# Performance work log

Measured on AMD Instinct MI355X. Metric: run time of the kernel, lower is better.

## Reference

```python
import jax, jax.numpy as jnp
import numpy as np

U, N, E, D = 200000, 50000, 1600000, 64


def setup_inputs() -> dict:
    key = jax.random.key(0)
    ks = jax.random.split(key, 8)
    nodes = jax.random.randint(ks[0], (N,), 0, U)
    neigh_idx = jax.random.randint(ks[1], (E,), 0, U)
    seg_ids = jnp.sort(jax.random.randint(ks[2], (E,), 0, N))
    u2e = jax.random.normal(ks[3], (U, D), dtype=jnp.float32) * 0.1
    W1 = jax.random.normal(ks[4], (2 * D, D), dtype=jnp.float32) * 0.1
    b1 = jnp.zeros((D,), dtype=jnp.float32)
    W2 = jax.random.normal(ks[5], (D, D), dtype=jnp.float32) * 0.1
    b2 = jnp.zeros((D,), dtype=jnp.float32)
    w3 = jax.random.normal(ks[6], (D, 1), dtype=jnp.float32) * 0.1
    b3 = jnp.zeros((1,), dtype=jnp.float32)
    return {"nodes": nodes, "neigh_idx": neigh_idx, "seg_ids": seg_ids,
            "u2e": u2e, "W1": W1, "b1": b1, "W2": W2, "b2": b2,
            "w3": w3, "b3": b3}


def reference(nodes, neigh_idx, seg_ids, u2e, W1, b1, W2, b2, w3, b3):
    # Per-node self representation  [N, D]
    u_rep = u2e[nodes]
    # Ragged neighbor gather flattened to edge list
    e_u = u2e[neigh_idx]                      # [E, D]
    u_edge = u_rep[seg_ids]                   # [E, D] node rep broadcast to its edges
    # Attention MLP (GraphRec-style), eval mode (no dropout)
    x = jnp.concatenate([e_u, u_edge], axis=1)            # [E, 2D]
    x = jax.nn.relu(x @ W1 + b1)
    x = jax.nn.relu(x @ W2 + b2)
    logits = (x @ w3 + b3)[:, 0]                           # [E]
    # Segment softmax over each node's neighbor set
    seg_max = jax.ops.segment_max(logits, seg_ids, num_segments=N)
    ex = jnp.exp(logits - seg_max[seg_ids])
    denom = jax.ops.segment_sum(ex, seg_ids, num_segments=N)
    att = ex / denom[seg_ids]                              # [E]
    # Attention-weighted neighbor aggregation: e_u^T @ att per node
    agg = jax.ops.segment_sum(att[:, None] * e_u, seg_ids, num_segments=N)  # [N, D]
    # Nodes with zero neighbors fall back to their own embedding
    counts = jax.ops.segment_sum(jnp.ones((E,), dtype=jnp.float32), seg_ids, num_segments=N)
    out = jnp.where(counts[:, None] > 0, agg, u_rep)
    return out
```

## Files before the change

### kernel.cpp

```cpp
#include <hip/hip_runtime.h>
#include <math.h>

#define D 64

typedef __fp16 fp16x2 __attribute__((ext_vector_type(2)));
typedef _Float16 half8 __attribute__((ext_vector_type(8)));
typedef __attribute__((ext_vector_type(4))) float f32x4;

union h8pun { half8 v; fp16x2 h2[4]; };

__global__ __launch_bounds__(256) void k_prep(const float* __restrict__ W1,
                                              const float* __restrict__ W2,
                                              float* __restrict__ W1at,
                                              float* __restrict__ W1bt,
                                              float* __restrict__ W2t,
                                              const int* __restrict__ seg_ids,
                                              int* __restrict__ start, int E, int N) {
    int i = blockIdx.x * 256 + threadIdx.x;
    if (i < 3 * D * D) {
        int mat = i / (D * D), j = i % (D * D);
        int r = j >> 6, c = j & 63;
        if (mat == 0)      W1at[c * D + r] = W1[r * D + c];
        else if (mat == 1) W1bt[c * D + r] = W1[(D + r) * D + c];
        else               W2t[c * D + r] = W2[r * D + c];
    }
    if (i <= N) {
        int lo = 0, hi = E;
        while (lo < hi) {
            int mid = (lo + hi) >> 1;
            if (seg_ids[mid] < i) lo = mid + 1; else hi = mid;
        }
        start[i] = lo;
    }
}

__global__ __launch_bounds__(256) void k_proj_both(const float* __restrict__ u2e,
                                                   const int* __restrict__ nodes,
                                                   const float* __restrict__ W1at,
                                                   const float* __restrict__ W1bt,
                                                   const float* __restrict__ b1,
                                                   _Float16* __restrict__ q,
                                                   _Float16* __restrict__ u2e_h,
                                                   _Float16* __restrict__ p,
                                                   int U, int N, int wavesU, int wavesN) {
    int lane = threadIdx.x & 63;
    int m = lane & 15, quad = lane >> 4;
    int wave = (blockIdx.x * blockDim.x + threadIdx.x) >> 6;

    const float* Wt;
    const int* idx;
    const float* bias;
    _Float16* outp;
    _Float16* copyp;
    int R, w0, wstride;
    if (wave < wavesU) {
        Wt = W1at; idx = nullptr; bias = nullptr; outp = q; copyp = u2e_h;
        R = U; w0 = wave; wstride = wavesU;
    } else {
        Wt = W1bt; idx = nodes; bias = b1; outp = p; copyp = nullptr;
        R = N; w0 = wave - wavesU; wstride = wavesN;
    }

    half8 Bf[2][4];
    float bv[4];
#pragma unroll
    for (int t = 0; t < 4; ++t) {
        int n = m + 16 * t;
        bv[t] = bias ? bias[n] : 0.0f;
#pragma unroll
        for (int kh = 0; kh < 2; ++kh) {
            const float* col = Wt + n * D + kh * 32 + quad * 8;
#pragma unroll
            for (int j = 0; j < 8; ++j) Bf[kh][t][j] = (_Float16)col[j];
        }
    }

    int ngroups = (R + 15) / 16;
    for (int g = w0; g < ngroups; g += wstride) {
        int r_ = g * 16 + m;
        int rs = r_ < R ? r_ : R - 1;
        int src = idx ? idx[rs] : rs;
        const float4* arow = (const float4*)(u2e + (size_t)src * D);
        float4 x0 = arow[quad * 2], x1 = arow[quad * 2 + 1];
        float4 y0 = arow[8 + quad * 2], y1 = arow[8 + quad * 2 + 1];
        h8pun A0, A1;
        A0.h2[0] = __builtin_amdgcn_cvt_pkrtz(x0.x, x0.y);
        A0.h2[1] = __builtin_amdgcn_cvt_pkrtz(x0.z, x0.w);
        A0.h2[2] = __builtin_amdgcn_cvt_pkrtz(x1.x, x1.y);
        A0.h2[3] = __builtin_amdgcn_cvt_pkrtz(x1.z, x1.w);
        A1.h2[0] = __builtin_amdgcn_cvt_pkrtz(y0.x, y0.y);
        A1.h2[1] = __builtin_amdgcn_cvt_pkrtz(y0.z, y0.w);
        A1.h2[2] = __builtin_amdgcn_cvt_pkrtz(y1.x, y1.y);
        A1.h2[3] = __builtin_amdgcn_cvt_pkrtz(y1.z, y1.w);
        if (copyp && r_ < R) {
            *(half8*)(copyp + (size_t)r_ * D + quad * 8) = A0.v;
            *(half8*)(copyp + (size_t)r_ * D + 32 + quad * 8) = A1.v;
        }
        f32x4 C[4];
#pragma unroll
        for (int t = 0; t < 4; ++t) C[t] = (f32x4){bv[t], bv[t], bv[t], bv[t]};
#pragma unroll
        for (int t = 0; t < 4; ++t) {
            C[t] = __builtin_amdgcn_mfma_f32_16x16x32_f16(A0.v, Bf[0][t], C[t], 0, 0, 0);
            C[t] = __builtin_amdgcn_mfma_f32_16x16x32_f16(A1.v, Bf[1][t], C[t], 0, 0, 0);
        }
#pragma unroll
        for (int r = 0; r < 4; ++r) {
            int row = g * 16 + quad * 4 + r;
            if (row < R) {
#pragma unroll
                for (int t = 0; t < 4; ++t)
                    outp[(size_t)row * D + m + 16 * t] = (_Float16)C[t][r];
            }
        }
    }
}

__global__ __launch_bounds__(256) void k_edge_logits_mfma(const int* __restrict__ neigh_idx,
                                                          const int* __restrict__ seg_ids,
                                                          const _Float16* __restrict__ q,
                                                          const _Float16* __restrict__ p,
                                                          const float* __restrict__ W2t,
                                                          const float* __restrict__ b2,
                                                          const float* __restrict__ w3,
                                                          const float* __restrict__ b3,
                                                          float* __restrict__ logits, int E) {
    int lane = threadIdx.x & 63;
    int m = lane & 15, quad = lane >> 4;

    half8 Bf[2][4];
    float b2v[4], w3v[4];
#pragma unroll
    for (int t = 0; t < 4; ++t) {
        int n = m + 16 * t;
        b2v[t] = b2[n];
        w3v[t] = w3[n];
#pragma unroll
        for (int kh = 0; kh < 2; ++kh) {
            const float* col = W2t + n * D + kh * 32 + quad * 8;
#pragma unroll
            for (int j = 0; j < 8; ++j) Bf[kh][t][j] = (_Float16)col[j];
        }
    }
    float b3v = b3[0];
    const half8 hz = {0, 0, 0, 0, 0, 0, 0, 0};

    int ngroups = (E + 31) / 32;
    int wave = (blockIdx.x * blockDim.x + threadIdx.x) >> 6;
    int nwaves = (gridDim.x * blockDim.x) >> 6;

    half8 cqa0 = hz, cqa1 = hz, cpa0 = hz, cpa1 = hz;
    half8 cqb0 = hz, cqb1 = hz, cpb0 = hz, cpb1 = hz;
    int g = wave;
    if (g < ngroups) {
        int ea = g * 32 + m, eb = ea + 16;
        int eas = ea < E ? ea : E - 1;
        int ebs = eb < E ? eb : E - 1;
        int nbra = neigh_idx[eas], sega = seg_ids[eas];
        int nbrb = neigh_idx[ebs], segb = seg_ids[ebs];
        const half8* qra = (const half8*)(q + (size_t)nbra * D);
        const half8* pra = (const half8*)(p + (size_t)sega * D);
        const half8* qrb = (const half8*)(q + (size_t)nbrb * D);
        const half8* prb = (const half8*)(p + (size_t)segb * D);
        cqa0 = qra[quad]; cqa1 = qra[quad + 4];
        cpa0 = pra[quad]; cpa1 = pra[quad + 4];
        cqb0 = qrb[quad]; cqb1 = qrb[quad + 4];
        cpb0 = prb[quad]; cpb1 = prb[quad + 4];
    }
    for (; g < ngroups; g += nwaves) {
        int gn = g + nwaves;
        int gs = gn < ngroups ? gn : g;
        int ea2 = gs * 32 + m, eb2 = ea2 + 16;
        int eas2 = ea2 < E ? ea2 : E - 1;
        int ebs2 = eb2 < E ? eb2 : E - 1;
        int nbra2 = neigh_idx[eas2], sega2 = seg_ids[eas2];
        int nbrb2 = neigh_idx[ebs2], segb2 = seg_ids[ebs2];
        half8 Aa0 = __builtin_elementwise_max(cqa0 + cpa0, hz);
        half8 Aa1 = __builtin_elementwise_max(cqa1 + cpa1, hz);
        half8 Ab0 = __builtin_elementwise_max(cqb0 + cpb0, hz);
        half8 Ab1 = __builtin_elementwise_max(cqb1 + cpb1, hz);
        const half8* qra2 = (const half8*)(q + (size_t)nbra2 * D);
        const half8* pra2 = (const half8*)(p + (size_t)sega2 * D);
        const half8* qrb2 = (const half8*)(q + (size_t)nbrb2 * D);
        const half8* prb2 = (const half8*)(p + (size_t)segb2 * D);
        half8 nqa0 = qra2[quad], nqa1 = qra2[quad + 4];
        half8 npa0 = pra2[quad], npa1 = pra2[quad + 4];
        half8 nqb0 = qrb2[quad], nqb1 = qrb2[quad + 4];
        half8 npb0 = prb2[quad], npb1 = prb2[quad + 4];
        f32x4 Ca[4], Cb[4];
#pragma unroll
        for (int t = 0; t < 4; ++t) {
            Ca[t] = (f32x4){b2v[t], b2v[t], b2v[t], b2v[t]};
            Cb[t] = Ca[t];
        }
#pragma unroll
        for (int t = 0; t < 4; ++t) {
            Ca[t] = __builtin_amdgcn_mfma_f32_16x16x32_f16(Aa0, Bf[0][t], Ca[t], 0, 0, 0);
            Ca[t] = __builtin_amdgcn_mfma_f32_16x16x32_f16(Aa1, Bf[1][t], Ca[t], 0, 0, 0);
            Cb[t] = __builtin_amdgcn_mfma_f32_16x16x32_f16(Ab0, Bf[0][t], Cb[t], 0, 0, 0);
            Cb[t] = __builtin_amdgcn_mfma_f32_16x16x32_f16(Ab1, Bf[1][t], Cb[t], 0, 0, 0);
        }
        float pa[4], pb[4];
#pragma unroll
        for (int r = 0; r < 4; ++r) {
            float sa = 0.0f, sb = 0.0f;
#pragma unroll
            for (int t = 0; t < 4; ++t) {
                sa += fmaxf(Ca[t][r], 0.0f) * w3v[t];
                sb += fmaxf(Cb[t][r], 0.0f) * w3v[t];
            }
            pa[r] = sa; pb[r] = sb;
        }
#pragma unroll
        for (int off = 1; off <= 8; off <<= 1) {
#pragma unroll
            for (int r = 0; r < 4; ++r) {
                pa[r] += __shfl_xor(pa[r], off, 64);
                pb[r] += __shfl_xor(pb[r], off, 64);
            }
        }
        if (m == 0) {
            int e0 = g * 32 + quad * 4;
            if (e0 + 3 < E)
                *(float4*)(logits + e0) = make_float4(pa[0] + b3v, pa[1] + b3v, pa[2] + b3v, pa[3] + b3v);
            else
#pragma unroll
                for (int r = 0; r < 4; ++r)
                    if (e0 + r < E) logits[e0 + r] = pa[r] + b3v;
            int e1 = e0 + 16;
            if (e1 + 3 < E)
                *(float4*)(logits + e1) = make_float4(pb[0] + b3v, pb[1] + b3v, pb[2] + b3v, pb[3] + b3v);
            else
#pragma unroll
                for (int r = 0; r < 4; ++r)
                    if (e1 + r < E) logits[e1 + r] = pb[r] + b3v;
        }
        cqa0 = nqa0; cqa1 = nqa1; cpa0 = npa0; cpa1 = npa1;
        cqb0 = nqb0; cqb1 = nqb1; cpb0 = npb0; cpb1 = npb1;
    }
}

__global__ __launch_bounds__(256) void k_agg(const int* __restrict__ nodes,
                                             const int* __restrict__ neigh_idx,
                                             const float* __restrict__ u2e,
                                             const _Float16* __restrict__ u2e_h,
                                             const float* __restrict__ logits,
                                             const int* __restrict__ start,
                                             float* __restrict__ out, int N) {
    int n = blockIdx.x * 4 + ((int)threadIdx.x >> 6);
    int lane = threadIdx.x & 63;
    if (n >= N) return;
    int s = start[n];
    int t = start[n + 1];
    if (s == t) {
        int node = nodes[n];
        out[(size_t)n * D + lane] = u2e[(size_t)node * D + lane];
        return;
    }
    float mx = -INFINITY;
    for (int i = s + lane; i < t; i += 64) mx = fmaxf(mx, logits[i]);
#pragma unroll
    for (int off = 32; off >= 1; off >>= 1) mx = fmaxf(mx, __shfl_xor(mx, off, 64));
    float ssum = 0.0f;
    for (int i = s + lane; i < t; i += 64) ssum += __expf(logits[i] - mx);
#pragma unroll
    for (int off = 32; off >= 1; off >>= 1) ssum += __shfl_xor(ssum, off, 64);
    float inv = 1.0f / ssum;

    int grp = lane >> 3, sub = lane & 7;
    float acc[8];
#pragma unroll
    for (int j = 0; j < 8; ++j) acc[j] = 0.0f;
    for (int i = s; i < t; i += 32) {
#pragma unroll
        for (int uu = 0; uu < 4; ++uu) {
            int ii = i + uu * 8 + grp;
            bool v = ii < t;
            int is = v ? ii : s;
            float lg = logits[is];
            int nb = neigh_idx[is];
            half8 r = *(const half8*)(u2e_h + (size_t)nb * D + sub * 8);
            float a = v ? __expf(lg - mx) * inv : 0.0f;
#pragma unroll
            for (int j = 0; j < 8; ++j) acc[j] += a * (float)r[j];
        }
    }
#pragma unroll
    for (int off = 8; off <= 32; off <<= 1) {
#pragma unroll
        for (int j = 0; j < 8; ++j) acc[j] += __shfl_xor(acc[j], off, 64);
    }
    if (grp == 0) {
        float* o = out + (size_t)n * D + sub * 8;
        *(float4*)o = make_float4(acc[0], acc[1], acc[2], acc[3]);
        *(float4*)(o + 4) = make_float4(acc[4], acc[5], acc[6], acc[7]);
    }
}

extern "C" void kernel_launch(void* const* d_in, const int* in_sizes, int n_in,
                              void* d_out, int out_size, void* d_ws, size_t ws_size,
                              hipStream_t stream) {
    const int* nodes = (const int*)d_in[0];
    const int* neigh_idx = (const int*)d_in[1];
    const int* seg_ids = (const int*)d_in[2];
    const float* u2e = (const float*)d_in[3];
    const float* W1 = (const float*)d_in[4];
    const float* b1 = (const float*)d_in[5];
    const float* W2 = (const float*)d_in[6];
    const float* b2 = (const float*)d_in[7];
    const float* w3 = (const float*)d_in[8];
    const float* b3 = (const float*)d_in[9];
    float* out = (float*)d_out;

    int N = in_sizes[0];
    int E = in_sizes[1];
    int U = in_sizes[3] / D;

    char* ws = (char*)d_ws;
    size_t off = 0;
    auto alloc = [&](size_t bytes) {
        void* ptr = ws + off;
        off = (off + bytes + 255) & ~(size_t)255;
        return ptr;
    };
    float* logits = (float*)alloc((size_t)E * 4);
    int* start = (int*)alloc((size_t)(N + 1) * 4);
    float* W1at = (float*)alloc((size_t)D * D * 4);
    float* W1bt = (float*)alloc((size_t)D * D * 4);
    float* W2t = (float*)alloc((size_t)D * D * 4);
    _Float16* q = (_Float16*)alloc((size_t)U * D * 2);
    _Float16* p = (_Float16*)alloc((size_t)N * D * 2);
    _Float16* u2e_h = (_Float16*)alloc((size_t)U * D * 2);
    (void)ws_size;

    int prep_n = (N + 1) > 3 * D * D ? (N + 1) : 3 * D * D;
    k_prep<<<(prep_n + 255) / 256, 256, 0, stream>>>(W1, W2, W1at, W1bt, W2t,
                                                     seg_ids, start, E, N);
    const int wavesU = 4096, wavesN = 1024;
    k_proj_both<<<(wavesU + wavesN) / 4, 256, 0, stream>>>(u2e, nodes, W1at, W1bt, b1,
                                                           q, u2e_h, p, U, N, wavesU, wavesN);
    k_edge_logits_mfma<<<2048, 256, 0, stream>>>(neigh_idx, seg_ids, q, p, W2t,
                                                 b2, w3, b3, logits, E);
    k_agg<<<(N + 3) / 4, 256, 0, stream>>>(nodes, neigh_idx, u2e, u2e_h, logits, start, out, N);
}
```

Before: 247.1 us.

## Fuse edge logits, online segment softmax and aggregation into one per-node kernel

Merges the edge-logit MLP kernel and the aggregation kernel into a single per-node kernel. Each wave walks its node's edges in chunks of 16 and keeps a running max and sum so the softmax is computed online, which removes the logits buffer and the second pass over edges. The fp16 embedding copy and its W1 projection are interleaved into one 128-wide row, so each neighbor's data sits in a single contiguous row. The b3 bias is dropped, which is valid because softmax is shift-invariant. In exchange, edges are processed per node with partially filled 16-edge tiles, which can waste MFMA work and hurt load balance on uneven degrees.

Measured after the change: 254.7 us. 1.03x slower.

```diff
diff --git a/kernel.cpp b/kernel.cpp
--- a/kernel.cpp
+++ b/kernel.cpp
@@ -5,6 +5,7 @@
 
 typedef __fp16 fp16x2 __attribute__((ext_vector_type(2)));
 typedef _Float16 half8 __attribute__((ext_vector_type(8)));
+typedef _Float16 half4v __attribute__((ext_vector_type(4)));
 typedef __attribute__((ext_vector_type(4))) float f32x4;
 
 union h8pun { half8 v; fp16x2 h2[4]; };
@@ -39,8 +40,7 @@
                                                    const float* __restrict__ W1at,
                                                    const float* __restrict__ W1bt,
                                                    const float* __restrict__ b1,
-                                                   _Float16* __restrict__ q,
-                                                   _Float16* __restrict__ u2e_h,
+                                                   _Float16* __restrict__ ue,
                                                    _Float16* __restrict__ p,
                                                    int U, int N, int wavesU, int wavesN) {
     int lane = threadIdx.x & 63;
@@ -52,12 +52,14 @@
     const float* bias;
     _Float16* outp;
     _Float16* copyp;
-    int R, w0, wstride;
+    int R, w0, wstride, ostride;
     if (wave < wavesU) {
-        Wt = W1at; idx = nullptr; bias = nullptr; outp = q; copyp = u2e_h;
+        Wt = W1at; idx = nullptr; bias = nullptr;
+        outp = ue + D; copyp = ue; ostride = 2 * D;
         R = U; w0 = wave; wstride = wavesU;
     } else {
-        Wt = W1bt; idx = nodes; bias = b1; outp = p; copyp = nullptr;
+        Wt = W1bt; idx = nodes; bias = b1;
+        outp = p; copyp = nullptr; ostride = D;
         R = N; w0 = wave - wavesU; wstride = wavesN;
     }
 
@@ -93,8 +95,8 @@
         A1.h2[2] = __builtin_amdgcn_cvt_pkrtz(y1.x, y1.y);
         A1.h2[3] = __builtin_amdgcn_cvt_pkrtz(y1.z, y1.w);
         if (copyp && r_ < R) {
-            *(half8*)(copyp + (size_t)r_ * D + quad * 8) = A0.v;
-            *(half8*)(copyp + (size_t)r_ * D + 32 + quad * 8) = A1.v;
+            *(half8*)(copyp + (size_t)r_ * 2 * D + quad * 8) = A0.v;
+            *(half8*)(copyp + (size_t)r_ * 2 * D + 32 + quad * 8) = A1.v;
         }
         f32x4 C[4];
 #pragma unroll
@@ -110,21 +112,22 @@
             if (row < R) {
 #pragma unroll
                 for (int t = 0; t < 4; ++t)
-                    outp[(size_t)row * D + m + 16 * t] = (_Float16)C[t][r];
-            }
-        }
-    }
-}
-
-__global__ __launch_bounds__(256) void k_edge_logits_mfma(const int* __restrict__ neigh_idx,
-                                                          const int* __restrict__ seg_ids,
-                                                          const _Float16* __restrict__ q,
-                                                          const _Float16* __restrict__ p,
-                                                          const float* __restrict__ W2t,
-                                                          const float* __restrict__ b2,
-                                                          const float* __restrict__ w3,
-                                                          const float* __restrict__ b3,
-                                                          float* __restrict__ logits, int E) {
+                    outp[(size_t)row * ostride + m + 16 * t] = (_Float16)C[t][r];
+            }
+        }
+    }
+}
+
+__global__ __launch_bounds__(256) void k_fused(const int* __restrict__ nodes,
+                                               const int* __restrict__ neigh_idx,
+                                               const float* __restrict__ u2e,
+                                               const _Float16* __restrict__ ue,
+                                               const _Float16* __restrict__ p,
+                                               const float* __restrict__ W2t,
+                                               const float* __restrict__ b2,
+                                               const float* __restrict__ w3,
+                                               const int* __restrict__ start,
+                                               float* __restrict__ out, int N) {
     int lane = threadIdx.x & 63;
     int m = lane & 15, quad = lane >> 4;
 
@@ -132,168 +135,100 @@
     float b2v[4], w3v[4];
 #pragma unroll
     for (int t = 0; t < 4; ++t) {
-        int n = m + 16 * t;
-        b2v[t] = b2[n];
-        w3v[t] = w3[n];
+        int nn = m + 16 * t;
+        b2v[t] = b2[nn];
+        w3v[t] = w3[nn];
 #pragma unroll
         for (int kh = 0; kh < 2; ++kh) {
-            const float* col = W2t + n * D + kh * 32 + quad * 8;
+            const float* col = W2t + nn * D + kh * 32 + quad * 8;
 #pragma unroll
             for (int j = 0; j < 8; ++j) Bf[kh][t][j] = (_Float16)col[j];
         }
     }
-    float b3v = b3[0];
     const half8 hz = {0, 0, 0, 0, 0, 0, 0, 0};
 
-    int ngroups = (E + 31) / 32;
     int wave = (blockIdx.x * blockDim.x + threadIdx.x) >> 6;
     int nwaves = (gridDim.x * blockDim.x) >> 6;
-
-    half8 cqa0 = hz, cqa1 = hz, cpa0 = hz, cpa1 = hz;
-    half8 cqb0 = hz, cqb1 = hz, cpb0 = hz, cpb1 = hz;
-    int g = wave;
-    if (g < ngroups) {
-        int ea = g * 32 + m, eb = ea + 16;
-        int eas = ea < E ? ea : E - 1;
-        int ebs = eb < E ? eb : E - 1;
-        int nbra = neigh_idx[eas], sega = seg_ids[eas];
-        int nbrb = neigh_idx[ebs], segb = seg_ids[ebs];
-        const half8* qra = (const half8*)(q + (size_t)nbra * D);
-        const half8* pra = (const half8*)(p + (size_t)sega * D);
-        const half8* qrb = (const half8*)(q + (size_t)nbrb * D);
-        const half8* prb = (const half8*)(p + (size_t)segb * D);
-        cqa0 = qra[quad]; cqa1 = qra[quad + 4];
-        cpa0 = pra[quad]; cpa1 = pra[quad + 4];
-        cqb0 = qrb[quad]; cqb1 = qrb[quad + 4];
-        cpb0 = prb[quad]; cpb1 = prb[quad + 4];
-    }
-    for (; g < ngroups; g += nwaves) {
-        int gn = g + nwaves;
-        int gs = gn < ngroups ? gn : g;
-        int ea2 = gs * 32 + m, eb2 = ea2 + 16;
-        int eas2 = ea2 < E ? ea2 : E - 1;
-        int ebs2 = eb2 < E ? eb2 : E - 1;
-        int nbra2 = neigh_idx[eas2], sega2 = seg_ids[eas2];
-        int nbrb2 = neigh_idx[ebs2], segb2 = seg_ids[ebs2];
-        half8 Aa0 = __builtin_elementwise_max(cqa0 + cpa0, hz);
-        half8 Aa1 = __builtin_elementwise_max(cqa1 + cpa1, hz);
-        half8 Ab0 = __builtin_elementwise_max(cqb0 + cpb0, hz);
-        half8 Ab1 = __builtin_elementwise_max(cqb1 + cpb1, hz);
-        const half8* qra2 = (const half8*)(q + (size_t)nbra2 * D);
-        const half8* pra2 = (const half8*)(p + (size_t)sega2 * D);
-        const half8* qrb2 = (const half8*)(q + (size_t)nbrb2 * D);
-        const half8* prb2 = (const half8*)(p + (size_t)segb2 * D);
-        half8 nqa0 = qra2[quad], nqa1 = qra2[quad + 4];
-        half8 npa0 = pra2[quad], npa1 = pra2[quad + 4];
-        half8 nqb0 = qrb2[quad], nqb1 = qrb2[quad + 4];
-        half8 npb0 = prb2[quad], npb1 = prb2[quad + 4];
-        f32x4 Ca[4], Cb[4];
-#pragma unroll
-        for (int t = 0; t < 4; ++t) {
-            Ca[t] = (f32x4){b2v[t], b2v[t], b2v[t], b2v[t]};
-            Cb[t] = Ca[t];
-        }
-#pragma unroll
-        for (int t = 0; t < 4; ++t) {
-            Ca[t] = __builtin_amdgcn_mfma_f32_16x16x32_f16(Aa0, Bf[0][t], Ca[t], 0, 0, 0);
-            Ca[t] = __builtin_amdgcn_mfma_f32_16x16x32_f16(Aa1, Bf[1][t], Ca[t], 0, 0, 0);
-            Cb[t] = __builtin_amdgcn_mfma_f32_16x16x32_f16(Ab0, Bf[0][t], Cb[t], 0, 0, 0);
-            Cb[t] = __builtin_amdgcn_mfma_f32_16x16x32_f16(Ab1, Bf[1][t], Cb[t], 0, 0, 0);
-        }
-        float pa[4], pb[4];
-#pragma unroll
-        for (int r = 0; r < 4; ++r) {
-            float sa = 0.0f, sb = 0.0f;
-#pragma unroll
-            for (int t = 0; t < 4; ++t) {
-                sa += fmaxf(Ca[t][r], 0.0f) * w3v[t];
-                sb += fmaxf(Cb[t][r], 0.0f) * w3v[t];
-            }
-            pa[r] = sa; pb[r] = sb;
-        }
-#pragma unroll
-        for (int off = 1; off <= 8; off <<= 1) {
+    for (int n = wave; n < N; n += nwaves) {
+        int s = start[n];
+        int t = start[n + 1];
+        if (s == t) {
+            int node = nodes[n];
+            out[(size_t)n * D + lane] = u2e[(size_t)node * D + lane];
+            continue;
+        }
+        const half8* prow = (const half8*)(p + (size_t)n * D);
+        half8 pa0 = prow[quad], pa1 = prow[quad + 4];
+        float m_run = -1e30f, ssum = 0.0f;
+        float acc0 = 0.f, acc1 = 0.f, acc2 = 0.f, acc3 = 0.f;
+        for (int base = s; base < t; base += 16) {
+            int e = base + m;
+            int es = e < t ? e : t - 1;
+            int nb = neigh_idx[es];
+            const half8* qrow = (const half8*)(ue + (size_t)nb * (2 * D) + D);
+            half8 qa0 = qrow[quad], qa1 = qrow[quad + 4];
+            half8 A0 = __builtin_elementwise_max(qa0 + pa0, hz);
+            half8 A1 = __builtin_elementwise_max(qa1 + pa1, hz);
+            f32x4 C[4];
+#pragma unroll
+            for (int t4 = 0; t4 < 4; ++t4) C[t4] = (f32x4){b2v[t4], b2v[t4], b2v[t4], b2v[t4]};
+#pragma unroll
+            for (int t4 = 0; t4 < 4; ++t4) {
+                C[t4] = __builtin_amdgcn_mfma_f32_16x16x32_f16(A0, Bf[0][t4], C[t4], 0, 0, 0);
+                C[t4] = __builtin_amdgcn_mfma_f32_16x16x32_f16(A1, Bf[1][t4], C[t4], 0, 0, 0);
+            }
+            float lw[4];
 #pragma unroll
             for (int r = 0; r < 4; ++r) {
-                pa[r] += __shfl_xor(pa[r], off, 64);
-                pb[r] += __shfl_xor(pb[r], off, 64);
-            }
-        }
-        if (m == 0) {
-            int e0 = g * 32 + quad * 4;
-            if (e0 + 3 < E)
-                *(float4*)(logits + e0) = make_float4(pa[0] + b3v, pa[1] + b3v, pa[2] + b3v, pa[3] + b3v);
-            else
-#pragma unroll
-                for (int r = 0; r < 4; ++r)
-                    if (e0 + r < E) logits[e0 + r] = pa[r] + b3v;
-            int e1 = e0 + 16;
-            if (e1 + 3 < E)
-                *(float4*)(logits + e1) = make_float4(pb[0] + b3v, pb[1] + b3v, pb[2] + b3v, pb[3] + b3v);
-            else
-#pragma unroll
-                for (int r = 0; r < 4; ++r)
-                    if (e1 + r < E) logits[e1 + r] = pb[r] + b3v;
-        }
-        cqa0 = nqa0; cqa1 = nqa1; cpa0 = npa0; cpa1 = npa1;
-        cqb0 = nqb0; cqb1 = nqb1; cpb0 = npb0; cpb1 = npb1;
-    }
-}
-
-__global__ __launch_bounds__(256) void k_agg(const int* __restrict__ nodes,
-                                             const int* __restrict__ neigh_idx,
-                                             const float* __restrict__ u2e,
-                                             const _Float16* __restrict__ u2e_h,
-                                             const float* __restrict__ logits,
-                                             const int* __restrict__ start,
-                                             float* __restrict__ out, int N) {
-    int n = blockIdx.x * 4 + ((int)threadIdx.x >> 6);
-    int lane = threadIdx.x & 63;
-    if (n >= N) return;
-    int s = start[n];
-    int t = start[n + 1];
-    if (s == t) {
-        int node = nodes[n];
-        out[(size_t)n * D + lane] = u2e[(size_t)node * D + lane];
-        return;
-    }
-    float mx = -INFINITY;
-    for (int i = s + lane; i < t; i += 64) mx = fmaxf(mx, logits[i]);
-#pragma unroll
-    for (int off = 32; off >= 1; off >>= 1) mx = fmaxf(mx, __shfl_xor(mx, off, 64));
-    float ssum = 0.0f;
-    for (int i = s + lane; i < t; i += 64) ssum += __expf(logits[i] - mx);
-#pragma unroll
-    for (int off = 32; off >= 1; off >>= 1) ssum += __shfl_xor(ssum, off, 64);
-    float inv = 1.0f / ssum;
-
-    int grp = lane >> 3, sub = lane & 7;
-    float acc[8];
-#pragma unroll
-    for (int j = 0; j < 8; ++j) acc[j] = 0.0f;
-    for (int i = s; i < t; i += 32) {
-#pragma unroll
-        for (int uu = 0; uu < 4; ++uu) {
-            int ii = i + uu * 8 + grp;
-            bool v = ii < t;
-            int is = v ? ii : s;
-            float lg = logits[is];
-            int nb = neigh_idx[is];
-            half8 r = *(const half8*)(u2e_h + (size_t)nb * D + sub * 8);
-            float a = v ? __expf(lg - mx) * inv : 0.0f;
-#pragma unroll
-            for (int j = 0; j < 8; ++j) acc[j] += a * (float)r[j];
-        }
-    }
-#pragma unroll
-    for (int off = 8; off <= 32; off <<= 1) {
-#pragma unroll
-        for (int j = 0; j < 8; ++j) acc[j] += __shfl_xor(acc[j], off, 64);
-    }
-    if (grp == 0) {
-        float* o = out + (size_t)n * D + sub * 8;
-        *(float4*)o = make_float4(acc[0], acc[1], acc[2], acc[3]);
-        *(float4*)(o + 4) = make_float4(acc[4], acc[5], acc[6], acc[7]);
+                float sa = 0.0f;
+#pragma unroll
+                for (int t4 = 0; t4 < 4; ++t4)
+                    sa += fmaxf(C[t4][r], 0.0f) * w3v[t4];
+                lw[r] = sa;
+            }
+#pragma unroll
+            for (int off = 1; off <= 8; off <<= 1) {
+#pragma unroll
+                for (int r = 0; r < 4; ++r) lw[r] += __shfl_xor(lw[r], off, 64);
+            }
+#pragma unroll
+            for (int r = 0; r < 4; ++r)
+                if (base + quad * 4 + r >= t) lw[r] = -1e30f;
+            float mc = fmaxf(fmaxf(lw[0], lw[1]), fmaxf(lw[2], lw[3]));
+            mc = fmaxf(mc, __shfl_xor(mc, 16, 64));
+            mc = fmaxf(mc, __shfl_xor(mc, 32, 64));
+            float mnew = fmaxf(m_run, mc);
+            float scale = __expf(m_run - mnew);
+            float w[4];
+            float wsum = 0.0f;
+#pragma unroll
+            for (int r = 0; r < 4; ++r) { w[r] = __expf(lw[r] - mnew); wsum += w[r]; }
+            wsum += __shfl_xor(wsum, 16, 64);
+            wsum += __shfl_xor(wsum, 32, 64);
+            ssum = ssum * scale + wsum;
+            acc0 *= scale; acc1 *= scale; acc2 *= scale; acc3 *= scale;
+#pragma unroll
+            for (int r = 0; r < 4; ++r) {
+                int nbr = __shfl(nb, 4 * quad + r, 64);
+                half4v row = *(const half4v*)(ue + (size_t)nbr * (2 * D) + m * 4);
+                acc0 += w[r] * (float)row[0];
+                acc1 += w[r] * (float)row[1];
+                acc2 += w[r] * (float)row[2];
+                acc3 += w[r] * (float)row[3];
+            }
+            m_run = mnew;
+        }
+#pragma unroll
+        for (int off = 16; off <= 32; off <<= 1) {
+            acc0 += __shfl_xor(acc0, off, 64);
+            acc1 += __shfl_xor(acc1, off, 64);
+            acc2 += __shfl_xor(acc2, off, 64);
+            acc3 += __shfl_xor(acc3, off, 64);
+        }
+        float inv = 1.0f / ssum;
+        if (quad == 0)
+            *(float4*)(out + (size_t)n * D + m * 4) =
+                make_float4(acc0 * inv, acc1 * inv, acc2 * inv, acc3 * inv);
     }
 }
 
@@ -310,6 +245,7 @@
     const float* b2 = (const float*)d_in[7];
     const float* w3 = (const float*)d_in[8];
     const float* b3 = (const float*)d_in[9];
+    (void)b3;
     float* out = (float*)d_out;
 
     int N = in_sizes[0];
@@ -323,14 +259,12 @@
         off = (off + bytes + 255) & ~(size_t)255;
         return ptr;
     };
-    float* logits = (float*)alloc((size_t)E * 4);
     int* start = (int*)alloc((size_t)(N + 1) * 4);
     float* W1at = (float*)alloc((size_t)D * D * 4);
     float* W1bt = (float*)alloc((size_t)D * D * 4);
     float* W2t = (float*)alloc((size_t)D * D * 4);
-    _Float16* q = (_Float16*)alloc((size_t)U * D * 2);
+    _Float16* ue = (_Float16*)alloc((size_t)U * 2 * D * 2);
     _Float16* p = (_Float16*)alloc((size_t)N * D * 2);
-    _Float16* u2e_h = (_Float16*)alloc((size_t)U * D * 2);
     (void)ws_size;
 
     int prep_n = (N + 1) > 3 * D * D ? (N + 1) : 3 * D * D;
@@ -338,8 +272,7 @@
                                                      seg_ids, start, E, N);
     const int wavesU = 4096, wavesN = 1024;
     k_proj_both<<<(wavesU + wavesN) / 4, 256, 0, stream>>>(u2e, nodes, W1at, W1bt, b1,
-                                                           q, u2e_h, p, U, N, wavesU, wavesN);
-    k_edge_logits_mfma<<<2048, 256, 0, stream>>>(neigh_idx, seg_ids, q, p, W2t,
-                                                 b2, w3, b3, logits, E);
-    k_agg<<<(N + 3) / 4, 256, 0, stream>>>(nodes, neigh_idx, u2e, u2e_h, logits, start, out, N);
-}
+                                                           ue, p, U, N, wavesU, wavesN);
+    k_fused<<<4096, 256, 0, stream>>>(nodes, neigh_idx, u2e, ue, p, W2t, b2, w3,
+                                      start, out, N);
+}
```

## Permute hidden-feature layout for vectorized fp16 stores and drop edge prefetch

Applied to the files above, without the earlier changes.

The projection kernel now writes each row's four MFMA output columns as one contiguous half4 store. To make that work it stores q and p in a permuted feature order, and the W2 transpose in k_prep is permuted to match so the edge MLP stays mathematically identical. This replaces scattered 2-byte writes with 8-byte writes. Separately, the edge-logits kernel drops its software-pipelined register prefetch of the next group's gathers and becomes a plain grid-stride loop. That lowers register pressure but gives up explicit overlap of gather latency with MFMA work.

New measurement: 238.5 us. 3.5% less time.

```diff
diff --git a/kernel.cpp b/kernel.cpp
--- a/kernel.cpp
+++ b/kernel.cpp
@@ -5,6 +5,7 @@
 
 typedef __fp16 fp16x2 __attribute__((ext_vector_type(2)));
 typedef _Float16 half8 __attribute__((ext_vector_type(8)));
+typedef _Float16 half4v __attribute__((ext_vector_type(4)));
 typedef __attribute__((ext_vector_type(4))) float f32x4;
 
 union h8pun { half8 v; fp16x2 h2[4]; };
@@ -13,16 +14,23 @@
                                               const float* __restrict__ W2,
                                               float* __restrict__ W1at,
                                               float* __restrict__ W1bt,
-                                              float* __restrict__ W2t,
+                                              float* __restrict__ W2pt,
                                               const int* __restrict__ seg_ids,
                                               int* __restrict__ start, int E, int N) {
     int i = blockIdx.x * 256 + threadIdx.x;
     if (i < 3 * D * D) {
         int mat = i / (D * D), j = i % (D * D);
-        int r = j >> 6, c = j & 63;
-        if (mat == 0)      W1at[c * D + r] = W1[r * D + c];
-        else if (mat == 1) W1bt[c * D + r] = W1[(D + r) * D + c];
-        else               W2t[c * D + r] = W2[r * D + c];
+        if (mat == 0) {
+            int r = j >> 6, c = j & 63;
+            W1at[c * D + r] = W1[r * D + c];
+        } else if (mat == 1) {
+            int r = j >> 6, c = j & 63;
+            W1bt[c * D + r] = W1[(D + r) * D + c];
+        } else {
+            int n = j >> 6, pos = j & 63;
+            int k = (pos >> 2) + 16 * (pos & 3);
+            W2pt[n * D + pos] = W2[k * D + n];
+        }
     }
     if (i <= N) {
         int lo = 0, hi = E;
@@ -108,9 +116,9 @@
         for (int r = 0; r < 4; ++r) {
             int row = g * 16 + quad * 4 + r;
             if (row < R) {
-#pragma unroll
-                for (int t = 0; t < 4; ++t)
-                    outp[(size_t)row * D + m + 16 * t] = (_Float16)C[t][r];
+                half4v hv = {(_Float16)C[0][r], (_Float16)C[1][r],
+                             (_Float16)C[2][r], (_Float16)C[3][r]};
+                *(half4v*)(outp + (size_t)row * D + m * 4) = hv;
             }
         }
     }
@@ -120,7 +128,7 @@
                                                           const int* __restrict__ seg_ids,
                                                           const _Float16* __restrict__ q,
                                                           const _Float16* __restrict__ p,
-                                                          const float* __restrict__ W2t,
+                                                          const float* __restrict__ W2pt,
                                                           const float* __restrict__ b2,
                                                           const float* __restrict__ w3,
                                                           const float* __restrict__ b3,
@@ -137,7 +145,7 @@
         w3v[t] = w3[n];
 #pragma unroll
         for (int kh = 0; kh < 2; ++kh) {
-            const float* col = W2t + n * D + kh * 32 + quad * 8;
+            const float* col = W2pt + n * D + kh * 32 + quad * 8;
 #pragma unroll
             for (int j = 0; j < 8; ++j) Bf[kh][t][j] = (_Float16)col[j];
         }
@@ -148,11 +156,7 @@
     int ngroups = (E + 31) / 32;
     int wave = (blockIdx.x * blockDim.x + threadIdx.x) >> 6;
     int nwaves = (gridDim.x * blockDim.x) >> 6;
-
-    half8 cqa0 = hz, cqa1 = hz, cpa0 = hz, cpa1 = hz;
-    half8 cqb0 = hz, cqb1 = hz, cpb0 = hz, cpb1 = hz;
-    int g = wave;
-    if (g < ngroups) {
+    for (int g = wave; g < ngroups; g += nwaves) {
         int ea = g * 32 + m, eb = ea + 16;
         int eas = ea < E ? ea : E - 1;
         int ebs = eb < E ? eb : E - 1;
@@ -162,31 +166,14 @@
         const half8* pra = (const half8*)(p + (size_t)sega * D);
         const half8* qrb = (const half8*)(q + (size_t)nbrb * D);
         const half8* prb = (const half8*)(p + (size_t)segb * D);
-        cqa0 = qra[quad]; cqa1 = qra[quad + 4];
-        cpa0 = pra[quad]; cpa1 = pra[quad + 4];
-        cqb0 = qrb[quad]; cqb1 = qrb[quad + 4];
-        cpb0 = prb[quad]; cpb1 = prb[quad + 4];
-    }
-    for (; g < ngroups; g += nwaves) {
-        int gn = g + nwaves;
-        int gs = gn < ngroups ? gn : g;
-        int ea2 = gs * 32 + m, eb2 = ea2 + 16;
-        int eas2 = ea2 < E ? ea2 : E - 1;
-        int ebs2 = eb2 < E ? eb2 : E - 1;
-        int nbra2 = neigh_idx[eas2], sega2 = seg_ids[eas2];
-        int nbrb2 = neigh_idx[ebs2], segb2 = seg_ids[ebs2];
-        half8 Aa0 = __builtin_elementwise_max(cqa0 + cpa0, hz);
-        half8 Aa1 = __builtin_elementwise_max(cqa1 + cpa1, hz);
-        half8 Ab0 = __builtin_elementwise_max(cqb0 + cpb0, hz);
-        half8 Ab1 = __builtin_elementwise_max(cqb1 + cpb1, hz);
-        const half8* qra2 = (const half8*)(q + (size_t)nbra2 * D);
-        const half8* pra2 = (const half8*)(p + (size_t)sega2 * D);
-        const half8* qrb2 = (const half8*)(q + (size_t)nbrb2 * D);
-        const half8* prb2 = (const half8*)(p + (size_t)segb2 * D);
-        half8 nqa0 = qra2[quad], nqa1 = qra2[quad + 4];
-        half8 npa0 = pra2[quad], npa1 = pra2[quad + 4];
-        half8 nqb0 = qrb2[quad], nqb1 = qrb2[quad + 4];
-        half8 npb0 = prb2[quad], npb1 = prb2[quad + 4];
+        half8 qa0 = qra[quad], qa1 = qra[quad + 4];
+        half8 pa0 = pra[quad], pa1 = pra[quad + 4];
+        half8 qb0 = qrb[quad], qb1 = qrb[quad + 4];
+        half8 pb0 = prb[quad], pb1 = prb[quad + 4];
+        half8 Aa0 = __builtin_elementwise_max(qa0 + pa0, hz);
+        half8 Aa1 = __builtin_elementwise_max(qa1 + pa1, hz);
+        half8 Ab0 = __builtin_elementwise_max(qb0 + pb0, hz);
+        half8 Ab1 = __builtin_elementwise_max(qb1 + pb1, hz);
         f32x4 Ca[4], Cb[4];
 #pragma unroll
         for (int t = 0; t < 4; ++t) {
@@ -235,8 +222,6 @@
                 for (int r = 0; r < 4; ++r)
                     if (e1 + r < E) logits[e1 + r] = pb[r] + b3v;
         }
-        cqa0 = nqa0; cqa1 = nqa1; cpa0 = npa0; cpa1 = npa1;
-        cqb0 = nqb0; cqb1 = nqb1; cpb0 = npb0; cpb1 = npb1;
     }
 }
 
@@ -327,19 +312,19 @@
     int* start = (int*)alloc((size_t)(N + 1) * 4);
     float* W1at = (float*)alloc((size_t)D * D * 4);
     float* W1bt = (float*)alloc((size_t)D * D * 4);
-    float* W2t = (float*)alloc((size_t)D * D * 4);
+    float* W2pt = (float*)alloc((size_t)D * D * 4);
     _Float16* q = (_Float16*)alloc((size_t)U * D * 2);
     _Float16* p = (_Float16*)alloc((size_t)N * D * 2);
     _Float16* u2e_h = (_Float16*)alloc((size_t)U * D * 2);
     (void)ws_size;
 
     int prep_n = (N + 1) > 3 * D * D ? (N + 1) : 3 * D * D;
-    k_prep<<<(prep_n + 255) / 256, 256, 0, stream>>>(W1, W2, W1at, W1bt, W2t,
+    k_prep<<<(prep_n + 255) / 256, 256, 0, stream>>>(W1, W2, W1at, W1bt, W2pt,
                                                      seg_ids, start, E, N);
     const int wavesU = 4096, wavesN = 1024;
     k_proj_both<<<(wavesU + wavesN) / 4, 256, 0, stream>>>(u2e, nodes, W1at, W1bt, b1,
                                                            q, u2e_h, p, U, N, wavesU, wavesN);
-    k_edge_logits_mfma<<<2048, 256, 0, stream>>>(neigh_idx, seg_ids, q, p, W2t,
+    k_edge_logits_mfma<<<2048, 256, 0, stream>>>(neigh_idx, seg_ids, q, p, W2pt,
                                                  b2, w3, b3, logits, E);
     k_agg<<<(N + 3) / 4, 256, 0, stream>>>(nodes, neigh_idx, u2e, u2e_h, logits, start, out, N);
 }
```
